# Kernel tuning notes

Measured on AMD Instinct MI355X. Metric: run time of the kernel, lower is better.

Reference implementation:

```python
import jax, jax.numpy as jnp
import numpy as np

SEQ_LEN = 4096
IN_DIM = 1024
QVK_DIM = 1024


def setup_inputs() -> dict:
    key = jax.random.key(0)
    kx, kw = jax.random.split(key)
    x = jax.random.normal(kx, (SEQ_LEN, IN_DIM), dtype=jnp.float32)
    # glorot-uniform-ish scale for W: limit = sqrt(6/(fan_in+fan_out))
    limit = np.sqrt(6.0 / (IN_DIM + 3 * QVK_DIM)).astype(np.float32)
    W = jax.random.uniform(kw, (IN_DIM, 3 * QVK_DIM), dtype=jnp.float32,
                           minval=-limit, maxval=limit)
    return {"x": x, "W": W}


def reference(x, W):
    seq_len = x.shape[0]
    qvk = x @ W                                   # [S, 3*D]
    # NOTE: original splits as queries, VALS, keys (vals is the middle chunk)
    queries, vals, keys = jnp.split(qvk, 3, axis=1)
    raw = (queries @ keys.T) / jnp.sqrt(jnp.float32(QVK_DIM))  # [S, S]
    # causal mask: strictly-upper-triangular entries -> -inf (same as the
    # original's scatter of -inf at triu_indices(seq_len, 1))
    causal = jnp.tril(jnp.ones((seq_len, seq_len), dtype=bool))
    raw = jnp.where(causal, raw, -jnp.inf)
    weights = jax.nn.softmax(raw, axis=1)
    return weights @ vals                         # [S, D]
```

## Files before the change

kernel.cpp:

```cpp
#include <hip/hip_runtime.h>

#define SEQ 4096
#define KDIM 1024
#define NQKV 3072
#define BK 32

typedef __bf16 bf16x8 __attribute__((ext_vector_type(8)));
typedef float  f32x4  __attribute__((ext_vector_type(4)));

#define WAITV(n) asm volatile("s_waitcnt vmcnt(" #n ")" ::: "memory")
#define BAR()    asm volatile("s_barrier" ::: "memory")

__device__ __forceinline__ unsigned short f2b(float f) {
    unsigned int u = __float_as_uint(f);
    u += 0x7FFFu + ((u >> 16) & 1u);
    return (unsigned short)(u >> 16);
}
__device__ __forceinline__ float b2f(unsigned short h) {
    return __uint_as_float(((unsigned int)h) << 16);
}

__device__ __forceinline__ void gld_lds16(const unsigned short* g, unsigned short* l) {
    __builtin_amdgcn_global_load_lds(
        (const __attribute__((address_space(1))) void*)g,
        (__attribute__((address_space(3))) void*)l, 16, 0, 0);
}

__device__ __forceinline__ void stage_tiles(
    const unsigned short* Ag, int lda, const unsigned short* Bg, int ldb,
    int k0, unsigned short* sA, unsigned short* sB, int wave, int lane)
{
    #pragma unroll
    for (int i = 0; i < 2; ++i) {
        int c = wave * 128 + i * 64 + lane;
        int row = c >> 2, slot = c & 3;
        int p = slot ^ ((row >> 1) & 3);
        gld_lds16(Ag + row * lda + k0 + p * 8, sA + (wave * 2 + i) * 512);
        gld_lds16(Bg + row * ldb + k0 + p * 8, sB + (wave * 2 + i) * 512);
    }
}

__device__ __forceinline__ const unsigned short* frag_addr(
    const unsigned short* s, int row, int quad)
{
    return s + row * 32 + (quad ^ ((row >> 1) & 3)) * 8;
}

__device__ __forceinline__ void compute_tile(
    const unsigned short* sA, const unsigned short* sB, f32x4 acc[4][4],
    int wm, int wn, int lr, int quad)
{
    bf16x8 af[4], bq[4];
    #pragma unroll
    for (int i = 0; i < 4; ++i)
        af[i] = *(const bf16x8*)frag_addr(sA, wm + 16 * i + lr, quad);
    #pragma unroll
    for (int j = 0; j < 4; ++j)
        bq[j] = *(const bf16x8*)frag_addr(sB, wn + 16 * j + lr, quad);
    #pragma unroll
    for (int i = 0; i < 4; ++i)
        #pragma unroll
        for (int j = 0; j < 4; ++j)
            acc[i][j] = __builtin_amdgcn_mfma_f32_16x16x32_bf16(af[i], bq[j], acc[i][j], 0, 0, 0);
}

__device__ __forceinline__ void mfma_pipe(
    const unsigned short* Ag, int lda, const unsigned short* Bg, int ldb,
    int kLen, unsigned short* lds, f32x4 acc[4][4])
{
    const int tid  = threadIdx.x;
    const int wave = tid >> 6, lane = tid & 63;
    const int lr   = lane & 15, quad = lane >> 4;
    const int wm   = (wave >> 1) * 64, wn = (wave & 1) * 64;
    const int niter = kLen >> 5;

    #pragma unroll
    for (int s = 0; s < 2; ++s)
        if (s < niter)
            stage_tiles(Ag, lda, Bg, ldb, s * BK,
                        lds + s * 8192, lds + s * 8192 + 4096, wave, lane);

    #pragma unroll 1
    for (int k = 0; k < niter; ++k) {
        if (k + 1 < niter) WAITV(4);
        else               WAITV(0);
        BAR();
        if (k + 2 < niter) {
            const int s = (k + 2) % 3;
            stage_tiles(Ag, lda, Bg, ldb, (k + 2) * BK,
                        lds + s * 8192, lds + s * 8192 + 4096, wave, lane);
        }
        const int c = k % 3;
        compute_tile(lds + c * 8192, lds + c * 8192 + 4096, acc, wm, wn, lr, quad);
    }
}

__device__ __forceinline__ void mfma_db(
    const unsigned short* Ag, int lda, const unsigned short* Bg, int ldb,
    int kLen, unsigned short* lds, f32x4 acc[4][4])
{
    const int tid  = threadIdx.x;
    const int wave = tid >> 6, lane = tid & 63;
    const int lr   = lane & 15, quad = lane >> 4;
    const int wm   = (wave >> 1) * 64, wn = (wave & 1) * 64;
    unsigned short* sA0 = lds;
    unsigned short* sB0 = lds + 4096;
    unsigned short* sA1 = lds + 8192;
    unsigned short* sB1 = lds + 12288;

    stage_tiles(Ag, lda, Bg, ldb, 0, sA0, sB0, wave, lane);
    int k = BK;
    #pragma unroll 1
    for (; k + BK < kLen; k += 2 * BK) {
        __syncthreads();
        stage_tiles(Ag, lda, Bg, ldb, k, sA1, sB1, wave, lane);
        compute_tile(sA0, sB0, acc, wm, wn, lr, quad);
        __syncthreads();
        stage_tiles(Ag, lda, Bg, ldb, k + BK, sA0, sB0, wave, lane);
        compute_tile(sA1, sB1, acc, wm, wn, lr, quad);
    }
    if (k < kLen) {
        __syncthreads();
        stage_tiles(Ag, lda, Bg, ldb, k, sA1, sB1, wave, lane);
        compute_tile(sA0, sB0, acc, wm, wn, lr, quad);
        __syncthreads();
        compute_tile(sA1, sB1, acc, wm, wn, lr, quad);
    } else {
        __syncthreads();
        compute_tile(sA0, sB0, acc, wm, wn, lr, quad);
    }
}

__device__ __forceinline__ void zero_acc(f32x4 acc[4][4]) {
    const f32x4 z = {0.f, 0.f, 0.f, 0.f};
    #pragma unroll
    for (int i = 0; i < 4; ++i)
        #pragma unroll
        for (int j = 0; j < 4; ++j) acc[i][j] = z;
}

__device__ __forceinline__ void store_rows_bf16(
    f32x4 acc[4][4], unsigned short* Cw, int ld, unsigned short* lw, int lane)
{
    const int lr = lane & 15, quad = lane >> 4;
    #pragma unroll
    for (int i = 0; i < 4; ++i) {
        #pragma unroll
        for (int j = 0; j < 4; ++j)
            #pragma unroll
            for (int r = 0; r < 4; ++r)
                lw[(quad * 4 + r) * 72 + j * 16 + lr] = f2b(acc[i][j][r]);
        #pragma unroll
        for (int t = 0; t < 2; ++t) {
            int chunk = t * 64 + lane;
            int rl = chunk >> 3, c8 = chunk & 7;
            uint4 v = *(const uint4*)(lw + rl * 72 + c8 * 8);
            *(uint4*)(Cw + (16 * i + rl) * ld + c8 * 8) = v;
        }
    }
}

__device__ __forceinline__ void store_cols_bf16(
    f32x4 acc[4][4], unsigned short* Vw, unsigned short* lw, int lane)
{
    const int lr = lane & 15, quad = lane >> 4;
    #pragma unroll
    for (int ip = 0; ip < 2; ++ip) {
        #pragma unroll
        for (int ii = 0; ii < 2; ++ii)
            #pragma unroll
            for (int j = 0; j < 4; ++j)
                #pragma unroll
                for (int r = 0; r < 4; ++r)
                    lw[(j * 16 + lr) * 40 + ii * 16 + quad * 4 + r] = f2b(acc[ip * 2 + ii][j][r]);
        #pragma unroll
        for (int t = 0; t < 4; ++t) {
            int chunk = t * 64 + lane;
            int col = chunk >> 2, c8 = chunk & 3;
            uint4 v = *(const uint4*)(lw + col * 40 + c8 * 8);
            *(uint4*)(Vw + col * SEQ + ip * 32 + c8 * 8) = v;
        }
    }
}

__global__ __launch_bounds__(256) void prep(
    const float* __restrict__ x, unsigned short* __restrict__ Xb,
    const float* __restrict__ W, unsigned short* __restrict__ Wt,
    float4* __restrict__ out, float4* __restrict__ lrow)
{
    __shared__ float tile[32][33];
    const int b = blockIdx.x, tid = threadIdx.x;
    if (b < 4096) {
        int i = (b * 256 + tid) * 4;
        float4 v = *(const float4*)(x + i);
        ushort4 o;
        o.x = f2b(v.x); o.y = f2b(v.y); o.z = f2b(v.z); o.w = f2b(v.w);
        *(ushort4*)(Xb + i) = o;
    } else if (b < 8192) {
        const float4 z = {0.f, 0.f, 0.f, 0.f};
        out[(b - 4096) * 256 + tid] = z;
    } else if (b < 11264) {
        const int bb = b - 8192;
        const int n0 = (bb % 96) * 32, k0 = (bb / 96) * 32;
        const int c = tid & 31, r0 = tid >> 5;
        #pragma unroll
        for (int r = r0; r < 32; r += 8)
            tile[r][c] = W[(k0 + r) * NQKV + n0 + c];
        __syncthreads();
        #pragma unroll
        for (int r = r0; r < 32; r += 8)
            Wt[(n0 + r) * KDIM + k0 + c] = f2b(tile[c][r]);
    } else {
        const float4 z = {0.f, 0.f, 0.f, 0.f};
        #pragma unroll
        for (int k = 0; k < 4; ++k) lrow[tid * 4 + k] = z;
    }
}

__global__ __launch_bounds__(256) void qvk_gemm(
    const unsigned short* __restrict__ Xb, const unsigned short* __restrict__ Wt,
    unsigned short* __restrict__ Qb, unsigned short* __restrict__ Kb,
    unsigned short* __restrict__ Vt)
{
    __shared__ __align__(16) unsigned short lds[24576];
    const int m0 = blockIdx.x * 128;
    const int n0 = blockIdx.y * 128;
    f32x4 acc[4][4];
    zero_acc(acc);
    mfma_pipe(Xb + m0 * KDIM, KDIM, Wt + n0 * KDIM, KDIM, KDIM, lds, acc);
    __syncthreads();

    const int lane = threadIdx.x & 63, wave = threadIdx.x >> 6;
    const int wm = (wave >> 1) * 64, wn = (wave & 1) * 64;
    unsigned short* lw = lds + wave * 2560;
    const int region = n0 >> 10;
    const int nloc = n0 & 1023;
    if (region == 0)
        store_rows_bf16(acc, Qb + (m0 + wm) * KDIM + nloc + wn, KDIM, lw, lane);
    else if (region == 2)
        store_rows_bf16(acc, Kb + (m0 + wm) * KDIM + nloc + wn, KDIM, lw, lane);
    else
        store_cols_bf16(acc, Vt + (nloc + wn) * SEQ + m0 + wm, lw, lane);
}

__global__ __launch_bounds__(256) void score_exp_gemm(
    const unsigned short* __restrict__ Qb, const unsigned short* __restrict__ Kb,
    unsigned short* __restrict__ Sb, float* __restrict__ lrow)
{
    __shared__ __align__(16) unsigned short lds[24576];
    const int bm = blockIdx.x, bn = blockIdx.y;
    if (bn > bm) return;
    const int m0 = bm * 128, n0 = bn * 128;

    f32x4 acc[4][4];
    zero_acc(acc);
    mfma_pipe(Qb + m0 * KDIM, KDIM, Kb + n0 * KDIM, KDIM, KDIM, lds, acc);

    const int lane = threadIdx.x & 63, wave = threadIdx.x >> 6;
    const int lr = lane & 15, quad = lane >> 4;
    const int wm = (wave >> 1) * 64, wn = (wave & 1) * 64;
    #pragma unroll
    for (int i = 0; i < 4; ++i)
        #pragma unroll
        for (int j = 0; j < 4; ++j)
            #pragma unroll
            for (int r = 0; r < 4; ++r) {
                float v = __expf(acc[i][j][r] * 0.03125f);
                if (bm == bn) {
                    int row = wm + 16 * i + quad * 4 + r;
                    int col = wn + 16 * j + lr;
                    if (col > row) v = 0.f;
                }
                acc[i][j][r] = v;
            }
    #pragma unroll
    for (int i = 0; i < 4; ++i)
        #pragma unroll
        for (int r = 0; r < 4; ++r) {
            float s = acc[i][0][r] + acc[i][1][r] + acc[i][2][r] + acc[i][3][r];
            s += __shfl_xor(s, 1, 16);
            s += __shfl_xor(s, 2, 16);
            s += __shfl_xor(s, 4, 16);
            s += __shfl_xor(s, 8, 16);
            if (lr == 0)
                atomicAdd(&lrow[m0 + wm + 16 * i + quad * 4 + r], s);
        }
    __syncthreads();
    store_rows_bf16(acc, Sb + (m0 + wm) * SEQ + n0 + wn, SEQ, lds + wave * 2560, lane);
}

__global__ __launch_bounds__(256) void pv_gemm(
    const unsigned short* __restrict__ Sb, const unsigned short* __restrict__ Vt,
    const float* __restrict__ lrow, float* __restrict__ out)
{
    __shared__ __align__(16) unsigned short lds[16384];
    const int n0 = blockIdx.x * 128;
    const int y = blockIdx.y;
    int m, c;
    if (y < 8)       { m = y;                 c = 0; }
    else if (y < 24) { m = 8 + (y - 8) / 2;   c = (y - 8) % 2; }
    else if (y < 48) { m = 16 + (y - 24) / 3; c = (y - 24) % 3; }
    else             { m = 24 + (y - 48) / 4; c = (y - 48) % 4; }
    const int m0 = m * 128;
    const int kstart = c * 1024;
    const int kend = min((m + 1) * 128, kstart + 1024);
    const int nchunks = (m >> 3) + 1;

    f32x4 acc[4][4];
    zero_acc(acc);
    mfma_db(Sb + m0 * SEQ + kstart, SEQ, Vt + n0 * SEQ + kstart, SEQ,
            kend - kstart, lds, acc);

    const int lane = threadIdx.x & 63, wave = threadIdx.x >> 6;
    const int lr = lane & 15, quad = lane >> 4;
    const int wm = (wave >> 1) * 64, wn = (wave & 1) * 64;
    #pragma unroll
    for (int i = 0; i < 4; ++i) {
        const int rbase = m0 + wm + 16 * i + quad * 4;
        const float4 l4 = *(const float4*)(lrow + rbase);
        float inv[4] = {1.0f / l4.x, 1.0f / l4.y, 1.0f / l4.z, 1.0f / l4.w};
        #pragma unroll
        for (int j = 0; j < 4; ++j) {
            const int col = n0 + wn + 16 * j + lr;
            if (nchunks == 1) {
                #pragma unroll
                for (int r = 0; r < 4; ++r)
                    out[(rbase + r) * KDIM + col] = acc[i][j][r] * inv[r];
            } else {
                #pragma unroll
                for (int r = 0; r < 4; ++r)
                    atomicAdd(&out[(rbase + r) * KDIM + col], acc[i][j][r] * inv[r]);
            }
        }
    }
}

extern "C" void kernel_launch(void* const* d_in, const int* in_sizes, int n_in,
                              void* d_out, int out_size, void* d_ws, size_t ws_size,
                              hipStream_t stream) {
    const float* x = (const float*)d_in[0];
    const float* W = (const float*)d_in[1];
    float* out = (float*)d_out;
    char* ws = (char*)d_ws;

    unsigned short* Xb = (unsigned short*)(ws);
    unsigned short* Wt = (unsigned short*)(ws + 8388608);
    unsigned short* Qb = (unsigned short*)(ws + 14680064);
    unsigned short* Kb = (unsigned short*)(ws + 23068672);
    unsigned short* Vt = (unsigned short*)(ws + 31457280);
    unsigned short* Sb = (unsigned short*)(ws + 39845888);
    float*        lrow = (float*)(ws + 73400320);

    prep          <<<11265, 256, 0, stream>>>(x, Xb, W, Wt, (float4*)out, (float4*)lrow);
    qvk_gemm      <<<dim3(SEQ / 128, NQKV / 128), 256, 0, stream>>>(Xb, Wt, Qb, Kb, Vt);
    score_exp_gemm<<<dim3(SEQ / 128, SEQ / 128), 256, 0, stream>>>(Qb, Kb, Sb, lrow);
    pv_gemm       <<<dim3(KDIM / 128, 80), 256, 0, stream>>>(Sb, Vt, lrow, out);
}
```

Baseline: 201.0 us.

## Enlarge GEMM block tiles to 256x256 with 8 waves and unify pipelined mainloop

Moves all three GEMMs from 128x128 tiles on 4 waves to 256x256 tiles on 8 waves, with each wave owning a 128x64 sub-tile (8x4 MFMA accumulators). The aim is higher operand reuse per LDS load and less global traffic per FLOP. pv_gemm drops its double-buffered loop and uses the shared triple-buffered pipeline, and its causal work split is remapped to the 256-row blocks. In exchange, register pressure roughly doubles, LDS per block grows to 96KB, grid sizes shrink (e.g. 40 blocks along y in pv), and causal masking now works at coarser 256-wide granularity, which adds wasted work.

```diff
diff --git a/kernel.cpp b/kernel.cpp
--- a/kernel.cpp
+++ b/kernel.cpp
@@ -32,11 +32,11 @@
 {
     #pragma unroll
     for (int i = 0; i < 2; ++i) {
-        int c = wave * 128 + i * 64 + lane;
+        int c = i * 512 + wave * 64 + lane;
         int row = c >> 2, slot = c & 3;
         int p = slot ^ ((row >> 1) & 3);
-        gld_lds16(Ag + row * lda + k0 + p * 8, sA + (wave * 2 + i) * 512);
-        gld_lds16(Bg + row * ldb + k0 + p * 8, sB + (wave * 2 + i) * 512);
+        gld_lds16(Ag + row * lda + k0 + p * 8, sA + (i * 8 + wave) * 512);
+        gld_lds16(Bg + row * ldb + k0 + p * 8, sB + (i * 8 + wave) * 512);
     }
 }
 
@@ -47,18 +47,18 @@
 }
 
 __device__ __forceinline__ void compute_tile(
-    const unsigned short* sA, const unsigned short* sB, f32x4 acc[4][4],
+    const unsigned short* sA, const unsigned short* sB, f32x4 acc[8][4],
     int wm, int wn, int lr, int quad)
 {
-    bf16x8 af[4], bq[4];
-    #pragma unroll
-    for (int i = 0; i < 4; ++i)
-        af[i] = *(const bf16x8*)frag_addr(sA, wm + 16 * i + lr, quad);
+    bf16x8 af[8], bq[4];
     #pragma unroll
     for (int j = 0; j < 4; ++j)
         bq[j] = *(const bf16x8*)frag_addr(sB, wn + 16 * j + lr, quad);
     #pragma unroll
-    for (int i = 0; i < 4; ++i)
+    for (int i = 0; i < 8; ++i)
+        af[i] = *(const bf16x8*)frag_addr(sA, wm + 16 * i + lr, quad);
+    #pragma unroll
+    for (int i = 0; i < 8; ++i)
         #pragma unroll
         for (int j = 0; j < 4; ++j)
             acc[i][j] = __builtin_amdgcn_mfma_f32_16x16x32_bf16(af[i], bq[j], acc[i][j], 0, 0, 0);
@@ -66,19 +66,19 @@
 
 __device__ __forceinline__ void mfma_pipe(
     const unsigned short* Ag, int lda, const unsigned short* Bg, int ldb,
-    int kLen, unsigned short* lds, f32x4 acc[4][4])
+    int kLen, unsigned short* lds, f32x4 acc[8][4])
 {
     const int tid  = threadIdx.x;
     const int wave = tid >> 6, lane = tid & 63;
     const int lr   = lane & 15, quad = lane >> 4;
-    const int wm   = (wave >> 1) * 64, wn = (wave & 1) * 64;
+    const int wm   = (wave >> 2) * 128, wn = (wave & 3) * 64;
     const int niter = kLen >> 5;
 
     #pragma unroll
     for (int s = 0; s < 2; ++s)
         if (s < niter)
             stage_tiles(Ag, lda, Bg, ldb, s * BK,
-                        lds + s * 8192, lds + s * 8192 + 4096, wave, lane);
+                        lds + s * 16384, lds + s * 16384 + 8192, wave, lane);
 
     #pragma unroll 1
     for (int k = 0; k < niter; ++k) {
@@ -88,63 +88,27 @@
         if (k + 2 < niter) {
             const int s = (k + 2) % 3;
             stage_tiles(Ag, lda, Bg, ldb, (k + 2) * BK,
-                        lds + s * 8192, lds + s * 8192 + 4096, wave, lane);
+                        lds + s * 16384, lds + s * 16384 + 8192, wave, lane);
         }
         const int c = k % 3;
-        compute_tile(lds + c * 8192, lds + c * 8192 + 4096, acc, wm, wn, lr, quad);
-    }
-}
-
-__device__ __forceinline__ void mfma_db(
-    const unsigned short* Ag, int lda, const unsigned short* Bg, int ldb,
-    int kLen, unsigned short* lds, f32x4 acc[4][4])
-{
-    const int tid  = threadIdx.x;
-    const int wave = tid >> 6, lane = tid & 63;
-    const int lr   = lane & 15, quad = lane >> 4;
-    const int wm   = (wave >> 1) * 64, wn = (wave & 1) * 64;
-    unsigned short* sA0 = lds;
-    unsigned short* sB0 = lds + 4096;
-    unsigned short* sA1 = lds + 8192;
-    unsigned short* sB1 = lds + 12288;
-
-    stage_tiles(Ag, lda, Bg, ldb, 0, sA0, sB0, wave, lane);
-    int k = BK;
-    #pragma unroll 1
-    for (; k + BK < kLen; k += 2 * BK) {
-        __syncthreads();
-        stage_tiles(Ag, lda, Bg, ldb, k, sA1, sB1, wave, lane);
-        compute_tile(sA0, sB0, acc, wm, wn, lr, quad);
-        __syncthreads();
-        stage_tiles(Ag, lda, Bg, ldb, k + BK, sA0, sB0, wave, lane);
-        compute_tile(sA1, sB1, acc, wm, wn, lr, quad);
-    }
-    if (k < kLen) {
-        __syncthreads();
-        stage_tiles(Ag, lda, Bg, ldb, k, sA1, sB1, wave, lane);
-        compute_tile(sA0, sB0, acc, wm, wn, lr, quad);
-        __syncthreads();
-        compute_tile(sA1, sB1, acc, wm, wn, lr, quad);
-    } else {
-        __syncthreads();
-        compute_tile(sA0, sB0, acc, wm, wn, lr, quad);
-    }
-}
-
-__device__ __forceinline__ void zero_acc(f32x4 acc[4][4]) {
+        compute_tile(lds + c * 16384, lds + c * 16384 + 8192, acc, wm, wn, lr, quad);
+    }
+}
+
+__device__ __forceinline__ void zero_acc(f32x4 acc[8][4]) {
     const f32x4 z = {0.f, 0.f, 0.f, 0.f};
     #pragma unroll
-    for (int i = 0; i < 4; ++i)
+    for (int i = 0; i < 8; ++i)
         #pragma unroll
         for (int j = 0; j < 4; ++j) acc[i][j] = z;
 }
 
 __device__ __forceinline__ void store_rows_bf16(
-    f32x4 acc[4][4], unsigned short* Cw, int ld, unsigned short* lw, int lane)
+    f32x4 acc[8][4], unsigned short* Cw, int ld, unsigned short* lw, int lane)
 {
     const int lr = lane & 15, quad = lane >> 4;
     #pragma unroll
-    for (int i = 0; i < 4; ++i) {
+    for (int i = 0; i < 8; ++i) {
         #pragma unroll
         for (int j = 0; j < 4; ++j)
             #pragma unroll
@@ -161,11 +125,11 @@
 }
 
 __device__ __forceinline__ void store_cols_bf16(
-    f32x4 acc[4][4], unsigned short* Vw, unsigned short* lw, int lane)
+    f32x4 acc[8][4], unsigned short* Vw, unsigned short* lw, int lane)
 {
     const int lr = lane & 15, quad = lane >> 4;
     #pragma unroll
-    for (int ip = 0; ip < 2; ++ip) {
+    for (int ip = 0; ip < 4; ++ip) {
         #pragma unroll
         for (int ii = 0; ii < 2; ++ii)
             #pragma unroll
@@ -217,21 +181,21 @@
     }
 }
 
-__global__ __launch_bounds__(256) void qvk_gemm(
+__global__ __launch_bounds__(512, 2) void qvk_gemm(
     const unsigned short* __restrict__ Xb, const unsigned short* __restrict__ Wt,
     unsigned short* __restrict__ Qb, unsigned short* __restrict__ Kb,
     unsigned short* __restrict__ Vt)
 {
-    __shared__ __align__(16) unsigned short lds[24576];
-    const int m0 = blockIdx.x * 128;
-    const int n0 = blockIdx.y * 128;
-    f32x4 acc[4][4];
+    __shared__ __align__(16) unsigned short lds[49152];
+    const int m0 = blockIdx.x * 256;
+    const int n0 = blockIdx.y * 256;
+    f32x4 acc[8][4];
     zero_acc(acc);
     mfma_pipe(Xb + m0 * KDIM, KDIM, Wt + n0 * KDIM, KDIM, KDIM, lds, acc);
     __syncthreads();
 
     const int lane = threadIdx.x & 63, wave = threadIdx.x >> 6;
-    const int wm = (wave >> 1) * 64, wn = (wave & 1) * 64;
+    const int wm = (wave >> 2) * 128, wn = (wave & 3) * 64;
     unsigned short* lw = lds + wave * 2560;
     const int region = n0 >> 10;
     const int nloc = n0 & 1023;
@@ -243,24 +207,24 @@
         store_cols_bf16(acc, Vt + (nloc + wn) * SEQ + m0 + wm, lw, lane);
 }
 
-__global__ __launch_bounds__(256) void score_exp_gemm(
+__global__ __launch_bounds__(512, 2) void score_exp_gemm(
     const unsigned short* __restrict__ Qb, const unsigned short* __restrict__ Kb,
     unsigned short* __restrict__ Sb, float* __restrict__ lrow)
 {
-    __shared__ __align__(16) unsigned short lds[24576];
+    __shared__ __align__(16) unsigned short lds[49152];
     const int bm = blockIdx.x, bn = blockIdx.y;
     if (bn > bm) return;
-    const int m0 = bm * 128, n0 = bn * 128;
-
-    f32x4 acc[4][4];
+    const int m0 = bm * 256, n0 = bn * 256;
+
+    f32x4 acc[8][4];
     zero_acc(acc);
     mfma_pipe(Qb + m0 * KDIM, KDIM, Kb + n0 * KDIM, KDIM, KDIM, lds, acc);
 
     const int lane = threadIdx.x & 63, wave = threadIdx.x >> 6;
     const int lr = lane & 15, quad = lane >> 4;
-    const int wm = (wave >> 1) * 64, wn = (wave & 1) * 64;
-    #pragma unroll
-    for (int i = 0; i < 4; ++i)
+    const int wm = (wave >> 2) * 128, wn = (wave & 3) * 64;
+    #pragma unroll
+    for (int i = 0; i < 8; ++i)
         #pragma unroll
         for (int j = 0; j < 4; ++j)
             #pragma unroll
@@ -274,7 +238,7 @@
                 acc[i][j][r] = v;
             }
     #pragma unroll
-    for (int i = 0; i < 4; ++i)
+    for (int i = 0; i < 8; ++i)
         #pragma unroll
         for (int r = 0; r < 4; ++r) {
             float s = acc[i][0][r] + acc[i][1][r] + acc[i][2][r] + acc[i][3][r];
@@ -289,33 +253,33 @@
     store_rows_bf16(acc, Sb + (m0 + wm) * SEQ + n0 + wn, SEQ, lds + wave * 2560, lane);
 }
 
-__global__ __launch_bounds__(256) void pv_gemm(
+__global__ __launch_bounds__(512, 2) void pv_gemm(
     const unsigned short* __restrict__ Sb, const unsigned short* __restrict__ Vt,
     const float* __restrict__ lrow, float* __restrict__ out)
 {
-    __shared__ __align__(16) unsigned short lds[16384];
-    const int n0 = blockIdx.x * 128;
+    __shared__ __align__(16) unsigned short lds[49152];
+    const int n0 = blockIdx.x * 256;
     const int y = blockIdx.y;
-    int m, c;
-    if (y < 8)       { m = y;                 c = 0; }
-    else if (y < 24) { m = 8 + (y - 8) / 2;   c = (y - 8) % 2; }
-    else if (y < 48) { m = 16 + (y - 24) / 3; c = (y - 24) % 3; }
-    else             { m = 24 + (y - 48) / 4; c = (y - 48) % 4; }
-    const int m0 = m * 128;
+    int mm, c;
+    if (y < 4)       { mm = y;                c = 0; }
+    else if (y < 12) { mm = 4 + (y - 4) / 2;  c = (y - 4) & 1; }
+    else if (y < 24) { mm = 8 + (y - 12) / 3; c = (y - 12) % 3; }
+    else             { mm = 12 + (y - 24) / 4; c = (y - 24) & 3; }
+    const int m0 = mm * 256;
     const int kstart = c * 1024;
-    const int kend = min((m + 1) * 128, kstart + 1024);
-    const int nchunks = (m >> 3) + 1;
-
-    f32x4 acc[4][4];
+    const int kend = min((mm + 1) * 256, kstart + 1024);
+    const int nchunks = (mm >> 2) + 1;
+
+    f32x4 acc[8][4];
     zero_acc(acc);
-    mfma_db(Sb + m0 * SEQ + kstart, SEQ, Vt + n0 * SEQ + kstart, SEQ,
-            kend - kstart, lds, acc);
+    mfma_pipe(Sb + m0 * SEQ + kstart, SEQ, Vt + n0 * SEQ + kstart, SEQ,
+              kend - kstart, lds, acc);
 
     const int lane = threadIdx.x & 63, wave = threadIdx.x >> 6;
     const int lr = lane & 15, quad = lane >> 4;
-    const int wm = (wave >> 1) * 64, wn = (wave & 1) * 64;
-    #pragma unroll
-    for (int i = 0; i < 4; ++i) {
+    const int wm = (wave >> 2) * 128, wn = (wave & 3) * 64;
+    #pragma unroll
+    for (int i = 0; i < 8; ++i) {
         const int rbase = m0 + wm + 16 * i + quad * 4;
         const float4 l4 = *(const float4*)(lrow + rbase);
         float inv[4] = {1.0f / l4.x, 1.0f / l4.y, 1.0f / l4.z, 1.0f / l4.w};
@@ -352,7 +316,7 @@
     float*        lrow = (float*)(ws + 73400320);
 
     prep          <<<11265, 256, 0, stream>>>(x, Xb, W, Wt, (float4*)out, (float4*)lrow);
-    qvk_gemm      <<<dim3(SEQ / 128, NQKV / 128), 256, 0, stream>>>(Xb, Wt, Qb, Kb, Vt);
-    score_exp_gemm<<<dim3(SEQ / 128, SEQ / 128), 256, 0, stream>>>(Qb, Kb, Sb, lrow);
-    pv_gemm       <<<dim3(KDIM / 128, 80), 256, 0, stream>>>(Sb, Vt, lrow, out);
-}
+    qvk_gemm      <<<dim3(SEQ / 256, NQKV / 256), 512, 0, stream>>>(Xb, Wt, Qb, Kb, Vt);
+    score_exp_gemm<<<dim3(SEQ / 256, SEQ / 256), 512, 0, stream>>>(Qb, Kb, Sb, lrow);
+    pv_gemm       <<<dim3(KDIM / 256, 40), 512, 0, stream>>>(Sb, Vt, lrow, out);
+}
```

Result: no change. 202.9 us (+0.9%).

## Use 256x256 eight-wave tiles with interleaved prefetch for QKV and score GEMMs

Applied to the files above, without the earlier changes.

Replaces the 128x128 four-wave GEMM pipeline in the QKV projection and score kernels with 256x256 tiles computed by eight waves. Loads are split into half-tile units and interleaved with MFMA phases, with s_setprio boosting the MFMA sections, so each byte fetched from global memory feeds more math. The score kernel now launches only the 136 lower-triangular blocks, using a triangular index decode instead of early-exiting upper blocks. Zeroing of out and lrow moves from the prep kernel to hipMemsetAsync. The trade-off is 128KB of LDS per block, more registers, fewer and larger blocks that may underfill the CUs, and a heavier load on the diagonal blocks.

```diff
diff --git a/kernel.cpp b/kernel.cpp
--- a/kernel.cpp
+++ b/kernel.cpp
@@ -10,15 +10,13 @@
 
 #define WAITV(n) asm volatile("s_waitcnt vmcnt(" #n ")" ::: "memory")
 #define BAR()    asm volatile("s_barrier" ::: "memory")
+#define SETP(n)  __builtin_amdgcn_s_setprio(n)
 
 __device__ __forceinline__ unsigned short f2b(float f) {
     unsigned int u = __float_as_uint(f);
     u += 0x7FFFu + ((u >> 16) & 1u);
     return (unsigned short)(u >> 16);
 }
-__device__ __forceinline__ float b2f(unsigned short h) {
-    return __uint_as_float(((unsigned int)h) << 16);
-}
 
 __device__ __forceinline__ void gld_lds16(const unsigned short* g, unsigned short* l) {
     __builtin_amdgcn_global_load_lds(
@@ -26,7 +24,235 @@
         (__attribute__((address_space(3))) void*)l, 16, 0, 0);
 }
 
-__device__ __forceinline__ void stage_tiles(
+__device__ __forceinline__ const unsigned short* frag_addr(
+    const unsigned short* s, int row, int quad)
+{
+    return s + row * 32 + (quad ^ ((row >> 1) & 3)) * 8;
+}
+
+__device__ __forceinline__ void stgU(
+    const unsigned short* G, int ldg, int tOff, int kk, int h,
+    unsigned short* unit, int tid)
+{
+    int row = tid >> 2, sl = tid & 3;
+    int p = sl ^ ((row >> 1) & 3);
+    gld_lds16(G + (h * 128 + row) * ldg + tOff + kk * 32 + p * 8,
+              unit + (tid >> 6) * 512);
+}
+
+__device__ __forceinline__ void rdA(
+    bf16x8 a[4], const unsigned short* u, int ih, int lr, int quad)
+{
+    #pragma unroll
+    for (int i = 0; i < 4; ++i)
+        a[i] = *(const bf16x8*)frag_addr(u, ih * 64 + 16 * i + lr, quad);
+}
+__device__ __forceinline__ void rdB(
+    bf16x8 b[4], const unsigned short* u, int bRow, int lr, int quad)
+{
+    #pragma unroll
+    for (int j = 0; j < 4; ++j)
+        b[j] = *(const bf16x8*)frag_addr(u, bRow + 16 * j + lr, quad);
+}
+__device__ __forceinline__ void mm8(
+    f32x4 acc[8][4], const bf16x8 a[4], const bf16x8 b[4], int io)
+{
+    #pragma unroll
+    for (int i = 0; i < 4; ++i)
+        #pragma unroll
+        for (int j = 0; j < 4; ++j)
+            acc[io + i][j] = __builtin_amdgcn_mfma_f32_16x16x32_bf16(
+                a[i], b[j], acc[io + i][j], 0, 0, 0);
+}
+
+__device__ __forceinline__ void mfma_pipe8(
+    const unsigned short* Ag, int lda, const unsigned short* Bg, int ldb,
+    unsigned short* lds, f32x4 acc[8][4])
+{
+    const int tid  = threadIdx.x;
+    const int wave = tid >> 6, lane = tid & 63;
+    const int lr   = lane & 15, quad = lane >> 4;
+    const int mg   = wave >> 2;
+    const int ng   = wave & 3;
+    const int hB   = ng >> 1, bRow = (ng & 1) * 64;
+    const int niter = 8;
+
+    const unsigned short* rA_d0k0 = lds + mg * 4096;
+    const unsigned short* rA_d0k1 = lds + 8192 + mg * 4096;
+    const unsigned short* rA_d1k0 = lds + 32768 + mg * 4096;
+    const unsigned short* rA_d1k1 = lds + 40960 + mg * 4096;
+    const unsigned short* rB_d0k0 = lds + 16384 + hB * 4096;
+    const unsigned short* rB_d0k1 = lds + 24576 + hB * 4096;
+    const unsigned short* rB_d1k0 = lds + 49152 + hB * 4096;
+    const unsigned short* rB_d1k1 = lds + 57344 + hB * 4096;
+
+    stgU(Ag, lda, 0, 0, 0, lds + 0,     tid);
+    stgU(Ag, lda, 0, 0, 1, lds + 4096,  tid);
+    stgU(Bg, ldb, 0, 0, 0, lds + 16384, tid);
+    stgU(Bg, ldb, 0, 0, 1, lds + 20480, tid);
+    stgU(Ag, lda, 0, 1, 0, lds + 8192,  tid);
+    stgU(Ag, lda, 0, 1, 1, lds + 12288, tid);
+    stgU(Bg, ldb, 0, 1, 0, lds + 24576, tid);
+    stgU(Bg, ldb, 0, 1, 1, lds + 28672, tid);
+    stgU(Ag, lda, 64, 0, 0, lds + 32768, tid);
+    stgU(Ag, lda, 64, 0, 1, lds + 36864, tid);
+    stgU(Bg, ldb, 64, 0, 0, lds + 49152, tid);
+    stgU(Bg, ldb, 64, 0, 1, lds + 53248, tid);
+    WAITV(4);
+    BAR();
+
+    bf16x8 a[4], b[4];
+
+    #pragma unroll 1
+    for (int u = 0; u < niter; ++u) {
+        const bool pre = (u + 1 < niter);
+        const int t1o = (2 * u + 1) * 64;
+        const int t2o = (2 * u + 2) * 64;
+        const int t3o = (2 * u + 3) * 64;
+
+        rdB(b, rB_d0k0, bRow, lr, quad);
+        rdA(a, rA_d0k0, 0, lr, quad);
+        stgU(Ag, lda, t1o, 1, 0, lds + 40960, tid);
+        stgU(Ag, lda, t1o, 1, 1, lds + 45056, tid);
+        BAR(); SETP(1); mm8(acc, a, b, 0); SETP(0); BAR();
+
+        rdA(a, rA_d0k0, 1, lr, quad);
+        stgU(Bg, ldb, t1o, 1, 0, lds + 57344, tid);
+        stgU(Bg, ldb, t1o, 1, 1, lds + 61440, tid);
+        BAR(); SETP(1); mm8(acc, a, b, 4); SETP(0); BAR();
+
+        rdB(b, rB_d0k1, bRow, lr, quad);
+        rdA(a, rA_d0k1, 0, lr, quad);
+        if (pre) {
+            stgU(Ag, lda, t2o, 0, 0, lds + 0,    tid);
+            stgU(Ag, lda, t2o, 0, 1, lds + 4096, tid);
+        }
+        BAR(); SETP(1); mm8(acc, a, b, 0); SETP(0); BAR();
+
+        rdA(a, rA_d0k1, 1, lr, quad);
+        if (pre) {
+            stgU(Bg, ldb, t2o, 0, 0, lds + 16384, tid);
+            stgU(Bg, ldb, t2o, 0, 1, lds + 20480, tid);
+        }
+        BAR(); SETP(1); mm8(acc, a, b, 4); SETP(0);
+        if (pre) WAITV(4); else WAITV(0);
+        BAR();
+
+        rdB(b, rB_d1k0, bRow, lr, quad);
+        rdA(a, rA_d1k0, 0, lr, quad);
+        if (pre) {
+            stgU(Ag, lda, t2o, 1, 0, lds + 8192,  tid);
+            stgU(Ag, lda, t2o, 1, 1, lds + 12288, tid);
+        }
+        BAR(); SETP(1); mm8(acc, a, b, 0); SETP(0); BAR();
+
+        rdA(a, rA_d1k0, 1, lr, quad);
+        if (pre) {
+            stgU(Bg, ldb, t2o, 1, 0, lds + 24576, tid);
+            stgU(Bg, ldb, t2o, 1, 1, lds + 28672, tid);
+        }
+        BAR(); SETP(1); mm8(acc, a, b, 4); SETP(0); BAR();
+
+        rdB(b, rB_d1k1, bRow, lr, quad);
+        rdA(a, rA_d1k1, 0, lr, quad);
+        if (pre) {
+            stgU(Ag, lda, t3o, 0, 0, lds + 32768, tid);
+            stgU(Ag, lda, t3o, 0, 1, lds + 36864, tid);
+        }
+        BAR(); SETP(1); mm8(acc, a, b, 0); SETP(0); BAR();
+
+        rdA(a, rA_d1k1, 1, lr, quad);
+        if (pre) {
+            stgU(Bg, ldb, t3o, 0, 0, lds + 49152, tid);
+            stgU(Bg, ldb, t3o, 0, 1, lds + 53248, tid);
+        }
+        BAR(); SETP(1); mm8(acc, a, b, 4); SETP(0);
+        if (pre) WAITV(4);
+        BAR();
+    }
+}
+
+__device__ __forceinline__ void zero_acc8(f32x4 acc[8][4]) {
+    const f32x4 z = {0.f, 0.f, 0.f, 0.f};
+    #pragma unroll
+    for (int i = 0; i < 8; ++i)
+        #pragma unroll
+        for (int j = 0; j < 4; ++j) acc[i][j] = z;
+}
+__device__ __forceinline__ void zero_acc4(f32x4 acc[4][4]) {
+    const f32x4 z = {0.f, 0.f, 0.f, 0.f};
+    #pragma unroll
+    for (int i = 0; i < 4; ++i)
+        #pragma unroll
+        for (int j = 0; j < 4; ++j) acc[i][j] = z;
+}
+
+__device__ __forceinline__ void store_rows8(
+    f32x4 acc[8][4], unsigned short* Cw, int ld, unsigned short* lw, int lane)
+{
+    const int lr = lane & 15, quad = lane >> 4;
+    #pragma unroll
+    for (int i = 0; i < 8; ++i) {
+        #pragma unroll
+        for (int j = 0; j < 4; ++j)
+            #pragma unroll
+            for (int r = 0; r < 4; ++r)
+                lw[(quad * 4 + r) * 72 + j * 16 + lr] = f2b(acc[i][j][r]);
+        #pragma unroll
+        for (int t = 0; t < 2; ++t) {
+            int chunk = t * 64 + lane;
+            int rl = chunk >> 3, c8 = chunk & 7;
+            uint4 v = *(const uint4*)(lw + rl * 72 + c8 * 8);
+            *(uint4*)(Cw + (16 * i + rl) * ld + c8 * 8) = v;
+        }
+    }
+}
+
+__device__ __forceinline__ void store_cols8(
+    f32x4 acc[8][4], unsigned short* Vw, unsigned short* lw, int lane)
+{
+    const int lr = lane & 15, quad = lane >> 4;
+    #pragma unroll
+    for (int ip = 0; ip < 4; ++ip) {
+        #pragma unroll
+        for (int ii = 0; ii < 2; ++ii)
+            #pragma unroll
+            for (int j = 0; j < 4; ++j)
+                #pragma unroll
+                for (int r = 0; r < 4; ++r)
+                    lw[(j * 16 + lr) * 40 + ii * 16 + quad * 4 + r] = f2b(acc[ip * 2 + ii][j][r]);
+        #pragma unroll
+        for (int t = 0; t < 4; ++t) {
+            int chunk = t * 64 + lane;
+            int col = chunk >> 2, c8 = chunk & 3;
+            uint4 v = *(const uint4*)(lw + col * 40 + c8 * 8);
+            *(uint4*)(Vw + col * SEQ + ip * 32 + c8 * 8) = v;
+        }
+    }
+}
+
+__device__ __forceinline__ void store_rows4(
+    f32x4 acc[4][4], unsigned short* Cw, int ld, unsigned short* lw, int lane)
+{
+    const int lr = lane & 15, quad = lane >> 4;
+    #pragma unroll
+    for (int i = 0; i < 4; ++i) {
+        #pragma unroll
+        for (int j = 0; j < 4; ++j)
+            #pragma unroll
+            for (int r = 0; r < 4; ++r)
+                lw[(quad * 4 + r) * 72 + j * 16 + lr] = f2b(acc[i][j][r]);
+        #pragma unroll
+        for (int t = 0; t < 2; ++t) {
+            int chunk = t * 64 + lane;
+            int rl = chunk >> 3, c8 = chunk & 7;
+            uint4 v = *(const uint4*)(lw + rl * 72 + c8 * 8);
+            *(uint4*)(Cw + (16 * i + rl) * ld + c8 * 8) = v;
+        }
+    }
+}
+
+__device__ __forceinline__ void stage_tiles4(
     const unsigned short* Ag, int lda, const unsigned short* Bg, int ldb,
     int k0, unsigned short* sA, unsigned short* sB, int wave, int lane)
 {
@@ -40,13 +266,7 @@
     }
 }
 
-__device__ __forceinline__ const unsigned short* frag_addr(
-    const unsigned short* s, int row, int quad)
-{
-    return s + row * 32 + (quad ^ ((row >> 1) & 3)) * 8;
-}
-
-__device__ __forceinline__ void compute_tile(
+__device__ __forceinline__ void compute_tile4(
     const unsigned short* sA, const unsigned short* sB, f32x4 acc[4][4],
     int wm, int wn, int lr, int quad)
 {
@@ -62,37 +282,6 @@
         #pragma unroll
         for (int j = 0; j < 4; ++j)
             acc[i][j] = __builtin_amdgcn_mfma_f32_16x16x32_bf16(af[i], bq[j], acc[i][j], 0, 0, 0);
-}
-
-__device__ __forceinline__ void mfma_pipe(
-    const unsigned short* Ag, int lda, const unsigned short* Bg, int ldb,
-    int kLen, unsigned short* lds, f32x4 acc[4][4])
-{
-    const int tid  = threadIdx.x;
-    const int wave = tid >> 6, lane = tid & 63;
-    const int lr   = lane & 15, quad = lane >> 4;
-    const int wm   = (wave >> 1) * 64, wn = (wave & 1) * 64;
-    const int niter = kLen >> 5;
-
-    #pragma unroll
-    for (int s = 0; s < 2; ++s)
-        if (s < niter)
-            stage_tiles(Ag, lda, Bg, ldb, s * BK,
-                        lds + s * 8192, lds + s * 8192 + 4096, wave, lane);
-
-    #pragma unroll 1
-    for (int k = 0; k < niter; ++k) {
-        if (k + 1 < niter) WAITV(4);
-        else               WAITV(0);
-        BAR();
-        if (k + 2 < niter) {
-            const int s = (k + 2) % 3;
-            stage_tiles(Ag, lda, Bg, ldb, (k + 2) * BK,
-                        lds + s * 8192, lds + s * 8192 + 4096, wave, lane);
-        }
-        const int c = k % 3;
-        compute_tile(lds + c * 8192, lds + c * 8192 + 4096, acc, wm, wn, lr, quad);
-    }
 }
 
 __device__ __forceinline__ void mfma_db(
@@ -108,85 +297,32 @@
     unsigned short* sA1 = lds + 8192;
     unsigned short* sB1 = lds + 12288;
 
-    stage_tiles(Ag, lda, Bg, ldb, 0, sA0, sB0, wave, lane);
+    stage_tiles4(Ag, lda, Bg, ldb, 0, sA0, sB0, wave, lane);
     int k = BK;
     #pragma unroll 1
     for (; k + BK < kLen; k += 2 * BK) {
         __syncthreads();
-        stage_tiles(Ag, lda, Bg, ldb, k, sA1, sB1, wave, lane);
-        compute_tile(sA0, sB0, acc, wm, wn, lr, quad);
-        __syncthreads();
-        stage_tiles(Ag, lda, Bg, ldb, k + BK, sA0, sB0, wave, lane);
-        compute_tile(sA1, sB1, acc, wm, wn, lr, quad);
+        stage_tiles4(Ag, lda, Bg, ldb, k, sA1, sB1, wave, lane);
+        compute_tile4(sA0, sB0, acc, wm, wn, lr, quad);
+        __syncthreads();
+        stage_tiles4(Ag, lda, Bg, ldb, k + BK, sA0, sB0, wave, lane);
+        compute_tile4(sA1, sB1, acc, wm, wn, lr, quad);
     }
     if (k < kLen) {
         __syncthreads();
-        stage_tiles(Ag, lda, Bg, ldb, k, sA1, sB1, wave, lane);
-        compute_tile(sA0, sB0, acc, wm, wn, lr, quad);
-        __syncthreads();
-        compute_tile(sA1, sB1, acc, wm, wn, lr, quad);
+        stage_tiles4(Ag, lda, Bg, ldb, k, sA1, sB1, wave, lane);
+        compute_tile4(sA0, sB0, acc, wm, wn, lr, quad);
+        __syncthreads();
+        compute_tile4(sA1, sB1, acc, wm, wn, lr, quad);
     } else {
         __syncthreads();
-        compute_tile(sA0, sB0, acc, wm, wn, lr, quad);
-    }
-}
-
-__device__ __forceinline__ void zero_acc(f32x4 acc[4][4]) {
-    const f32x4 z = {0.f, 0.f, 0.f, 0.f};
-    #pragma unroll
-    for (int i = 0; i < 4; ++i)
-        #pragma unroll
-        for (int j = 0; j < 4; ++j) acc[i][j] = z;
-}
-
-__device__ __forceinline__ void store_rows_bf16(
-    f32x4 acc[4][4], unsigned short* Cw, int ld, unsigned short* lw, int lane)
-{
-    const int lr = lane & 15, quad = lane >> 4;
-    #pragma unroll
-    for (int i = 0; i < 4; ++i) {
-        #pragma unroll
-        for (int j = 0; j < 4; ++j)
-            #pragma unroll
-            for (int r = 0; r < 4; ++r)
-                lw[(quad * 4 + r) * 72 + j * 16 + lr] = f2b(acc[i][j][r]);
-        #pragma unroll
-        for (int t = 0; t < 2; ++t) {
-            int chunk = t * 64 + lane;
-            int rl = chunk >> 3, c8 = chunk & 7;
-            uint4 v = *(const uint4*)(lw + rl * 72 + c8 * 8);
-            *(uint4*)(Cw + (16 * i + rl) * ld + c8 * 8) = v;
-        }
-    }
-}
-
-__device__ __forceinline__ void store_cols_bf16(
-    f32x4 acc[4][4], unsigned short* Vw, unsigned short* lw, int lane)
-{
-    const int lr = lane & 15, quad = lane >> 4;
-    #pragma unroll
-    for (int ip = 0; ip < 2; ++ip) {
-        #pragma unroll
-        for (int ii = 0; ii < 2; ++ii)
-            #pragma unroll
-            for (int j = 0; j < 4; ++j)
-                #pragma unroll
-                for (int r = 0; r < 4; ++r)
-                    lw[(j * 16 + lr) * 40 + ii * 16 + quad * 4 + r] = f2b(acc[ip * 2 + ii][j][r]);
-        #pragma unroll
-        for (int t = 0; t < 4; ++t) {
-            int chunk = t * 64 + lane;
-            int col = chunk >> 2, c8 = chunk & 3;
-            uint4 v = *(const uint4*)(lw + col * 40 + c8 * 8);
-            *(uint4*)(Vw + col * SEQ + ip * 32 + c8 * 8) = v;
-        }
+        compute_tile4(sA0, sB0, acc, wm, wn, lr, quad);
     }
 }
 
 __global__ __launch_bounds__(256) void prep(
     const float* __restrict__ x, unsigned short* __restrict__ Xb,
-    const float* __restrict__ W, unsigned short* __restrict__ Wt,
-    float4* __restrict__ out, float4* __restrict__ lrow)
+    const float* __restrict__ W, unsigned short* __restrict__ Wt)
 {
     __shared__ float tile[32][33];
     const int b = blockIdx.x, tid = threadIdx.x;
@@ -196,11 +332,8 @@
         ushort4 o;
         o.x = f2b(v.x); o.y = f2b(v.y); o.z = f2b(v.z); o.w = f2b(v.w);
         *(ushort4*)(Xb + i) = o;
-    } else if (b < 8192) {
-        const float4 z = {0.f, 0.f, 0.f, 0.f};
-        out[(b - 4096) * 256 + tid] = z;
-    } else if (b < 11264) {
-        const int bb = b - 8192;
+    } else {
+        const int bb = b - 4096;
         const int n0 = (bb % 96) * 32, k0 = (bb / 96) * 32;
         const int c = tid & 31, r0 = tid >> 5;
         #pragma unroll
@@ -210,57 +343,56 @@
         #pragma unroll
         for (int r = r0; r < 32; r += 8)
             Wt[(n0 + r) * KDIM + k0 + c] = f2b(tile[c][r]);
-    } else {
-        const float4 z = {0.f, 0.f, 0.f, 0.f};
-        #pragma unroll
-        for (int k = 0; k < 4; ++k) lrow[tid * 4 + k] = z;
-    }
-}
-
-__global__ __launch_bounds__(256) void qvk_gemm(
+    }
+}
+
+__global__ __launch_bounds__(512, 2) void qvk_gemm(
     const unsigned short* __restrict__ Xb, const unsigned short* __restrict__ Wt,
     unsigned short* __restrict__ Qb, unsigned short* __restrict__ Kb,
     unsigned short* __restrict__ Vt)
 {
-    __shared__ __align__(16) unsigned short lds[24576];
-    const int m0 = blockIdx.x * 128;
-    const int n0 = blockIdx.y * 128;
-    f32x4 acc[4][4];
-    zero_acc(acc);
-    mfma_pipe(Xb + m0 * KDIM, KDIM, Wt + n0 * KDIM, KDIM, KDIM, lds, acc);
+    __shared__ __align__(16) unsigned short lds[65536];
+    const int m0 = blockIdx.x * 256;
+    const int n0 = blockIdx.y * 256;
+    f32x4 acc[8][4];
+    zero_acc8(acc);
+    mfma_pipe8(Xb + m0 * KDIM, KDIM, Wt + n0 * KDIM, KDIM, lds, acc);
     __syncthreads();
 
     const int lane = threadIdx.x & 63, wave = threadIdx.x >> 6;
-    const int wm = (wave >> 1) * 64, wn = (wave & 1) * 64;
+    const int wm = (wave >> 2) * 128, wn = (wave & 3) * 64;
     unsigned short* lw = lds + wave * 2560;
     const int region = n0 >> 10;
     const int nloc = n0 & 1023;
     if (region == 0)
-        store_rows_bf16(acc, Qb + (m0 + wm) * KDIM + nloc + wn, KDIM, lw, lane);
+        store_rows8(acc, Qb + (m0 + wm) * KDIM + nloc + wn, KDIM, lw, lane);
     else if (region == 2)
-        store_rows_bf16(acc, Kb + (m0 + wm) * KDIM + nloc + wn, KDIM, lw, lane);
+        store_rows8(acc, Kb + (m0 + wm) * KDIM + nloc + wn, KDIM, lw, lane);
     else
-        store_cols_bf16(acc, Vt + (nloc + wn) * SEQ + m0 + wm, lw, lane);
-}
-
-__global__ __launch_bounds__(256) void score_exp_gemm(
+        store_cols8(acc, Vt + (nloc + wn) * SEQ + m0 + wm, lw, lane);
+}
+
+__global__ __launch_bounds__(512, 2) void score_exp_gemm(
     const unsigned short* __restrict__ Qb, const unsigned short* __restrict__ Kb,
     unsigned short* __restrict__ Sb, float* __restrict__ lrow)
 {
-    __shared__ __align__(16) unsigned short lds[24576];
-    const int bm = blockIdx.x, bn = blockIdx.y;
-    if (bn > bm) return;
-    const int m0 = bm * 128, n0 = bn * 128;
-
-    f32x4 acc[4][4];
-    zero_acc(acc);
-    mfma_pipe(Qb + m0 * KDIM, KDIM, Kb + n0 * KDIM, KDIM, KDIM, lds, acc);
+    __shared__ __align__(16) unsigned short lds[65536];
+    const int L = blockIdx.x;
+    int bm = (int)((sqrtf(8.0f * (float)L + 1.0f) - 1.0f) * 0.5f);
+    while ((bm + 1) * (bm + 2) / 2 <= L) ++bm;
+    while (bm * (bm + 1) / 2 > L) --bm;
+    const int bn = L - bm * (bm + 1) / 2;
+    const int m0 = bm * 256, n0 = bn * 256;
+
+    f32x4 acc[8][4];
+    zero_acc8(acc);
+    mfma_pipe8(Qb + m0 * KDIM, KDIM, Kb + n0 * KDIM, KDIM, lds, acc);
 
     const int lane = threadIdx.x & 63, wave = threadIdx.x >> 6;
     const int lr = lane & 15, quad = lane >> 4;
-    const int wm = (wave >> 1) * 64, wn = (wave & 1) * 64;
-    #pragma unroll
-    for (int i = 0; i < 4; ++i)
+    const int wm = (wave >> 2) * 128, wn = (wave & 3) * 64;
+    #pragma unroll
+    for (int i = 0; i < 8; ++i)
         #pragma unroll
         for (int j = 0; j < 4; ++j)
             #pragma unroll
@@ -274,7 +406,7 @@
                 acc[i][j][r] = v;
             }
     #pragma unroll
-    for (int i = 0; i < 4; ++i)
+    for (int i = 0; i < 8; ++i)
         #pragma unroll
         for (int r = 0; r < 4; ++r) {
             float s = acc[i][0][r] + acc[i][1][r] + acc[i][2][r] + acc[i][3][r];
@@ -286,7 +418,7 @@
                 atomicAdd(&lrow[m0 + wm + 16 * i + quad * 4 + r], s);
         }
     __syncthreads();
-    store_rows_bf16(acc, Sb + (m0 + wm) * SEQ + n0 + wn, SEQ, lds + wave * 2560, lane);
+    store_rows8(acc, Sb + (m0 + wm) * SEQ + n0 + wn, SEQ, lds + wave * 2560, lane);
 }
 
 __global__ __launch_bounds__(256) void pv_gemm(
@@ -307,7 +439,7 @@
     const int nchunks = (m >> 3) + 1;
 
     f32x4 acc[4][4];
-    zero_acc(acc);
+    zero_acc4(acc);
     mfma_db(Sb + m0 * SEQ + kstart, SEQ, Vt + n0 * SEQ + kstart, SEQ,
             kend - kstart, lds, acc);
 
@@ -351,8 +483,10 @@
     unsigned short* Sb = (unsigned short*)(ws + 39845888);
     float*        lrow = (float*)(ws + 73400320);
 
-    prep          <<<11265, 256, 0, stream>>>(x, Xb, W, Wt, (float4*)out, (float4*)lrow);
-    qvk_gemm      <<<dim3(SEQ / 128, NQKV / 128), 256, 0, stream>>>(Xb, Wt, Qb, Kb, Vt);
-    score_exp_gemm<<<dim3(SEQ / 128, SEQ / 128), 256, 0, stream>>>(Qb, Kb, Sb, lrow);
+    hipMemsetAsync(out, 0, (size_t)SEQ * KDIM * sizeof(float), stream);
+    hipMemsetAsync(lrow, 0, (size_t)SEQ * sizeof(float), stream);
+    prep          <<<7168, 256, 0, stream>>>(x, Xb, W, Wt);
+    qvk_gemm      <<<dim3(SEQ / 256, NQKV / 256), 512, 0, stream>>>(Xb, Wt, Qb, Kb, Vt);
+    score_exp_gemm<<<136, 512, 0, stream>>>(Qb, Kb, Sb, lrow);
     pv_gemm       <<<dim3(KDIM / 128, 80), 256, 0, stream>>>(Sb, Vt, lrow, out);
 }
```

Result: no change. 198.0 us (-1.5%).
